# Optimization experiments

Measured on AMD Instinct MI355X. Metric: run time of the kernel, lower is better.

The kernel has to match this reference:

```python
import jax, jax.numpy as jnp
import numpy as np

WH, WW = 7, 7
N = WH * WW
H = 16          # num_heads
D = 32          # head_dim
NW = 64         # num windows per image (mask.shape[0])


def _relative_position_index(wh, ww):
    coords = np.stack(np.meshgrid(np.arange(wh), np.arange(ww), indexing='ij'))  # (2, wh, ww)
    cf = coords.reshape(2, -1)                                                   # (2, N)
    rel = cf[:, :, None] - cf[:, None, :]                                        # (2, N, N)
    rel = rel.transpose(1, 2, 0).copy()
    rel[:, :, 0] += wh - 1
    rel[:, :, 1] += ww - 1
    rel[:, :, 0] *= 2 * ww - 1
    return rel.sum(-1)  # (N, N) int

REL_IDX = jnp.asarray(_relative_position_index(WH, WW))


def setup_inputs() -> dict:
    key = jax.random.key(0)
    ks = jax.random.split(key, 5)
    B_ = 2048
    dim = H * D
    x = jax.random.normal(ks[0], (B_, N, dim), dtype=jnp.float32)
    mask = jnp.zeros((NW, N, N), dtype=jnp.float32)
    rpb_table = jax.random.normal(ks[1], ((2 * WH - 1) * (2 * WW - 1), H), dtype=jnp.float32) * 0.02
    qkv_w = jax.random.normal(ks[2], (3 * dim, dim), dtype=jnp.float32) * (dim ** -0.5)
    qkv_b = jnp.zeros((3 * dim,), dtype=jnp.float32)
    proj_w = jax.random.normal(ks[3], (dim, dim), dtype=jnp.float32) * (dim ** -0.5)
    proj_b = jnp.zeros((dim,), dtype=jnp.float32)
    return {"x": x, "mask": mask, "rpb_table": rpb_table,
            "qkv_w": qkv_w, "qkv_b": qkv_b, "proj_w": proj_w, "proj_b": proj_b}


def reference(x, mask, rpb_table, qkv_w, qkv_b, proj_w, proj_b):
    B_, n, C = x.shape
    scale = D ** -0.5
    # qkv projection (torch Linear: x @ W^T + b)
    qkv = (x @ qkv_w.T + qkv_b).reshape(B_, n, 3, H, D)
    q = qkv[:, :, 0].transpose(0, 2, 1, 3) * scale  # (B_, H, N, D)
    k = qkv[:, :, 1].transpose(0, 2, 1, 3)
    v = qkv[:, :, 2].transpose(0, 2, 1, 3)
    attn = jnp.einsum('bhnd,bhmd->bhnm', q, k)      # (B_, H, N, N)
    # relative position bias: gather (N*N,) rows from table -> (N, N, H) -> (H, N, N)
    bias = rpb_table[REL_IDX.reshape(-1)].reshape(n, n, H).transpose(2, 0, 1)
    attn = attn + bias[None]
    # shifted-window mask add: (B, nW, H, N, N) + (1, nW, 1, N, N)
    nW = mask.shape[0]
    attn = attn.reshape(B_ // nW, nW, H, n, n) + mask[None, :, None]
    attn = attn.reshape(B_, H, n, n)
    attn = jax.nn.softmax(attn, axis=-1)
    out = jnp.einsum('bhnm,bhmd->bhnd', attn, v)    # (B_, H, N, D)
    out = out.transpose(0, 2, 1, 3).reshape(B_, n, H * D)
    return out @ proj_w.T + proj_b
```

## Files before the change

kernel.cpp:

```cpp
#include <hip/hip_runtime.h>

typedef _Float16 f16;
typedef _Float16 f16x8 __attribute__((ext_vector_type(8)));
typedef _Float16 f16x4 __attribute__((ext_vector_type(4)));
typedef __fp16 fp16x2 __attribute__((ext_vector_type(2)));
typedef float f32x4 __attribute__((ext_vector_type(4)));

#define NTOK 49
#define NH 16
#define HD 32
#define DIM 512
#define NWIN 64
#define NB 2048
#define MTOT (NB*NTOK)
#define SCALE 0.17677669529663687f
#define VTS 56

__device__ __forceinline__ void gload_lds16(const f16* g, f16* l) {
    __builtin_amdgcn_global_load_lds((const __attribute__((address_space(1))) void*)g,
                                     (__attribute__((address_space(3))) void*)l, 16, 0, 0);
}

__device__ __forceinline__ void cvt_body(const float* __restrict__ s, f16* __restrict__ d,
                                         int n4, int bid, int nb) {
    int i = bid * 256 + threadIdx.x;
    int st = nb * 256;
    for (; i < n4; i += st) {
        float4 v = ((const float4*)s)[i];
        f16x4 o = { (f16)v.x, (f16)v.y, (f16)v.z, (f16)v.w };
        *(f16x4*)(d + (size_t)i * 4) = o;
    }
}

__global__ __launch_bounds__(256) void prep_kernel(const float* __restrict__ rpb,
                                                   const float* __restrict__ mask,
                                                   f16* __restrict__ biasT,
                                                   f16* __restrict__ maskT,
                                                   const float* __restrict__ qkvw,
                                                   f16* __restrict__ w16,
                                                   const float* __restrict__ projw,
                                                   f16* __restrict__ pw16,
                                                   const float* __restrict__ x,
                                                   f16* __restrict__ x16) {
    const int bid = blockIdx.x;
    if (bid >= 1280) {
        if (bid < 1280 + 2048)      cvt_body(x, x16, MTOT * DIM / 4, bid - 1280, 2048);
        else if (bid < 1280 + 2816) cvt_body(qkvw, w16, 1536 * 512 / 4, bid - 1280 - 2048, 768);
        else                        cvt_body(projw, pw16, 512 * 512 / 4, bid - 1280 - 2816, 256);
        return;
    }
    const bool isBias = (bid < 256);
    int idx = (isBias ? bid : bid - 256) * 256 + threadIdx.x;
    int r  = idx & 3;
    int j  = (idx >> 2) & 3;
    int i  = (idx >> 4) & 3;
    int l  = (idx >> 6) & 63;
    int wh = idx >> 12;
    int g = l >> 4, c16 = l & 15;
    int k = i * 16 + g * 4 + r;
    int q = j * 16 + c16;
    float v;
    if (isBias) {
        if (k >= NTOK)      v = -30000.f;
        else if (q >= NTOK) v = 0.f;
        else {
            int rq = q / 7, cq = q - rq * 7;
            int rk = k / 7, ck = k - rk * 7;
            int rel = (rq - rk + 6) * 13 + (cq - ck + 6);
            v = rpb[rel * NH + wh];
        }
        biasT[idx] = (f16)v;
    } else {
        v = (k < NTOK && q < NTOK) ? mask[(wh * NTOK + q) * NTOK + k] : 0.f;
        maskT[idx] = (f16)v;
    }
}

#define WAIT_LGKM  asm volatile("s_waitcnt lgkmcnt(0)" ::: "memory")
#define WAIT_VM(N) asm volatile("s_waitcnt vmcnt(" #N ")" ::: "memory")

template<int NT>
__global__ __launch_bounds__(512) void gemm256(const f16* __restrict__ A,
                                               const f16* __restrict__ Bw,
                                               const float* __restrict__ bias,
                                               f16* __restrict__ qo,
                                               f16* __restrict__ ko,
                                               f16* __restrict__ vto) {
    __shared__ __align__(16) f16 As[2][256][64];
    __shared__ __align__(16) f16 Bs[2][256][64];

    const int tid = threadIdx.x;
    const int lane = tid & 63;
    const int wv = tid >> 6;
    const int wm = wv >> 2, wn = wv & 3;
    const int g = lane >> 4, c16 = lane & 15;

    const int nblk = gridDim.x;
    const int f = blockIdx.x;
    const int work = (f & 7) * (nblk >> 3) + (f >> 3);
    const int m0 = (work / NT) * 256;
    const int n0 = (work % NT) * 256;

    const int srow = lane >> 3;
    const int schunk = (lane & 7) ^ srow;
    const f16* gA = A  + (size_t)(m0 + wv * 16 + srow) * DIM + schunk * 8;
    const f16* gB = Bw + (size_t)(n0 + wv * 16 + srow) * DIM + schunk * 8;

#define STAGE1(buf, kt, role) do {                                             \
    const f16* _s = (((role) < 2) ? gA : gB) + (size_t)(((role) & 1) * 128) * DIM + (kt) * 64; \
    f16* _d = ((role) < 2) ? &As[buf][((role) & 1) * 128 + wv * 16][0]         \
                           : &Bs[buf][((role) & 1) * 128 + wv * 16][0];        \
    gload_lds16(_s, _d);                                                       \
    gload_lds16(_s + (size_t)8 * DIM, _d + 8 * 64);                            \
} while (0)
#define STAGE_T(buf, kt) do { STAGE1(buf, kt, 0); STAGE1(buf, kt, 1);          \
                              STAGE1(buf, kt, 2); STAGE1(buf, kt, 3); } while (0)

#define READS(buf, kk, AF, BF) do {                                            \
    _Pragma("unroll") for (int _i = 0; _i < 8; ++_i)                           \
        (AF)[_i] = *(const f16x8*)&As[buf][wm * 128 + _i * 16 + c16][(((kk) * 4 + g) ^ (c16 & 7)) * 8]; \
    _Pragma("unroll") for (int _j = 0; _j < 4; ++_j)                           \
        (BF)[_j] = *(const f16x8*)&Bs[buf][wn * 64 + _j * 16 + c16][(((kk) * 4 + g) ^ (c16 & 7)) * 8]; \
} while (0)

#define MM(AF, BF) do {                                                        \
    __builtin_amdgcn_s_setprio(1);                                             \
    _Pragma("unroll") for (int _j = 0; _j < 4; ++_j)                           \
    _Pragma("unroll") for (int _i = 0; _i < 8; ++_i)                           \
        acc[_j][_i] = __builtin_amdgcn_mfma_f32_16x16x32_f16((BF)[_j], (AF)[_i], acc[_j][_i], 0, 0, 0); \
    __builtin_amdgcn_s_setprio(0);                                             \
} while (0)

    f32x4 acc[4][8];
#pragma unroll
    for (int j = 0; j < 4; ++j)
#pragma unroll
        for (int i = 0; i < 8; ++i)
            acc[j][i] = (f32x4){0.f, 0.f, 0.f, 0.f};

    f16x8 a0[8], b0[4], a1[8], b1[4];

    const int KT = DIM / 64;

    STAGE_T(0, 0);
    STAGE_T(1, 1);
    WAIT_VM(8);
    __builtin_amdgcn_s_barrier();
    READS(0, 0, a0, b0);

#pragma unroll
    for (int t = 0; t < KT; ++t) {
        const int b = t & 1, nb = b ^ 1;

        READS(b, 1, a1, b1);
        MM(a0, b0);
        WAIT_LGKM;
        __builtin_amdgcn_s_barrier();
        if (t + 2 < KT) STAGE_T(b, t + 2);
        if (t + 2 < KT) { WAIT_VM(8); }
        else if (t + 1 < KT) { WAIT_VM(0); }

        if (t + 1 < KT) READS(nb, 0, a0, b0);
        MM(a1, b1);
    }
#undef STAGE1
#undef STAGE_T
#undef READS
#undef MM

#pragma unroll
    for (int i = 0; i < 8; ++i) {
        const int m = m0 + wm * 128 + i * 16 + c16;
        const int bb = m / NTOK, tk = m - (m / NTOK) * NTOK;
#pragma unroll
        for (int j = 0; j < 4; ++j) {
            const int n = n0 + wn * 64 + j * 16 + g * 4;
            f32x4 v = acc[j][i];
            const f32x4 b4 = *(const f32x4*)&bias[n];
            v += b4;
            const int s = n >> 9;
            const int hh = (n >> 5) & 15;
            const int d0 = n & 31;
            const size_t bh = (size_t)(bb * NH + hh);
            if (s == 0) {
                f16x4 o = { (f16)(v[0] * SCALE), (f16)(v[1] * SCALE),
                            (f16)(v[2] * SCALE), (f16)(v[3] * SCALE) };
                *(f16x4*)(qo + (bh * NTOK + tk) * HD + d0) = o;
            } else if (s == 1) {
                f16x4 o = { (f16)v[0], (f16)v[1], (f16)v[2], (f16)v[3] };
                *(f16x4*)(ko + (bh * NTOK + tk) * HD + d0) = o;
            } else {
#pragma unroll
                for (int r = 0; r < 4; ++r)
                    vto[(bh * HD + d0 + r) * VTS + tk] = (f16)v[r];
            }
        }
    }
}

__global__ __launch_bounds__(256, 3) void gemm128(const f16* __restrict__ A,
                                                  const f16* __restrict__ Bw,
                                                  const float* __restrict__ bias,
                                                  float* __restrict__ outp) {
    __shared__ __align__(16) f16 As[3][128][32];
    __shared__ __align__(16) f16 Bs[3][128][32];

    const int NT = 4;
    const int tid = threadIdx.x;
    const int lane = tid & 63;
    const int wv = tid >> 6;
    const int wr = wv >> 1, wc = wv & 1;
    const int g = lane >> 4, c16 = lane & 15;
    const int rsw = (c16 >> 1) & 3;

    const int nblk = gridDim.x;
    const int f = blockIdx.x;
    const int work = (f & 7) * (nblk >> 3) + (f >> 3);
    const int m0 = (work / NT) * 128;
    const int n0 = (work % NT) * 128;

    const int srow = lane >> 2;
    const int schunk = (lane & 3) ^ ((srow >> 1) & 3);
    const f16* gA = A  + (size_t)(m0 + wv * 32 + srow) * DIM + schunk * 8;
    const f16* gB = Bw + (size_t)(n0 + wv * 32 + srow) * DIM + schunk * 8;

#define STAGE6(buf, t) do { \
    gload_lds16(gA + (t) * 32,                     &As[buf][wv * 32][0]);      \
    gload_lds16(gA + (size_t)16 * DIM + (t) * 32,  &As[buf][wv * 32 + 16][0]); \
    gload_lds16(gB + (t) * 32,                     &Bs[buf][wv * 32][0]);      \
    gload_lds16(gB + (size_t)16 * DIM + (t) * 32,  &Bs[buf][wv * 32 + 16][0]); \
} while (0)

    f32x4 acc[4][4];
#pragma unroll
    for (int j = 0; j < 4; ++j)
#pragma unroll
        for (int i = 0; i < 4; ++i)
            acc[j][i] = (f32x4){0.f, 0.f, 0.f, 0.f};

    STAGE6(0, 0);
    STAGE6(1, 1);
    WAIT_VM(4);
    __builtin_amdgcn_s_barrier();

    const int KS = DIM / 32;
#pragma unroll
    for (int t = 0; t < KS; ++t) {
        const int cb = t % 3;
        if (t + 2 < KS) STAGE6((t + 2) % 3, t + 2);
        f16x8 af[4], bf[4];
#pragma unroll
        for (int i = 0; i < 4; ++i)
            af[i] = *(const f16x8*)&As[cb][wr * 64 + i * 16 + c16][(g ^ rsw) * 8];
#pragma unroll
        for (int j = 0; j < 4; ++j)
            bf[j] = *(const f16x8*)&Bs[cb][wc * 64 + j * 16 + c16][(g ^ rsw) * 8];
        __builtin_amdgcn_s_setprio(1);
#pragma unroll
        for (int j = 0; j < 4; ++j)
#pragma unroll
            for (int i = 0; i < 4; ++i)
                acc[j][i] = __builtin_amdgcn_mfma_f32_16x16x32_f16(bf[j], af[i], acc[j][i], 0, 0, 0);
        __builtin_amdgcn_s_setprio(0);
        WAIT_LGKM;
        __builtin_amdgcn_sched_barrier(0);
        if (t + 2 < KS) {
            WAIT_VM(4);
        } else if (t + 1 < KS) {
            WAIT_VM(0);
        }
        if (t + 1 < KS) __builtin_amdgcn_s_barrier();
    }
#undef STAGE6

#pragma unroll
    for (int i = 0; i < 4; ++i) {
        const int m = m0 + wr * 64 + i * 16 + c16;
#pragma unroll
        for (int j = 0; j < 4; ++j) {
            const int n = n0 + wc * 64 + j * 16 + g * 4;
            f32x4 v = acc[j][i];
            const f32x4 b4 = *(const f32x4*)&bias[n];
            v += b4;
            float4 o = { v[0], v[1], v[2], v[3] };
            *(float4*)(outp + (size_t)m * DIM + n) = o;
        }
    }
}

__global__ __launch_bounds__(256) void attn_kernel(const f16* __restrict__ qw,
                                                   const f16* __restrict__ kw,
                                                   const f16* __restrict__ vt,
                                                   const f16* __restrict__ biasT,
                                                   const f16* __restrict__ maskT,
                                                   f16* __restrict__ aout) {
    __shared__ __align__(16) f16 Ps[4][64][72];

    const int wv = threadIdx.x >> 6;
    const int l = threadIdx.x & 63;
    const int f = blockIdx.x;
    const int work = (f & 7) * (gridDim.x >> 3) + (f >> 3);
    const int bid = work * 4 + wv;
    const int b = bid >> 4, h = bid & 15;
    const int w = b & (NWIN - 1);
    const int g = l >> 4, c16 = l & 15;
    const size_t qkbase = (size_t)bid * (NTOK * HD);
    const size_t vbase = (size_t)bid * (HD * VTS);

    const f16x8 z8 = {};

    f16x8 qf[4], kf[4];
#pragma unroll
    for (int t = 0; t < 4; ++t) {
        int row = t * 16 + c16;
        f16x8 q = z8, k = z8;
        if (row < NTOK) {
            q = *(const f16x8*)(qw + qkbase + row * HD + g * 8);
            k = *(const f16x8*)(kw + qkbase + row * HD + g * 8);
        }
        qf[t] = q; kf[t] = k;
    }

    const f16* cbB = biasT + (((size_t)h * 64 + l) << 6);
    const f16* cbM = maskT + (((size_t)w * 64 + l) << 6);
    f16x8 cbv[8];
#pragma unroll
    for (int k = 0; k < 8; ++k)
        cbv[k] = *(const f16x8*)(cbB + k * 8) + *(const f16x8*)(cbM + k * 8);
    f32x4 St[4][4];
#pragma unroll
    for (int i = 0; i < 4; ++i)
#pragma unroll
        for (int j = 0; j < 4; ++j) {
            const int e = i * 16 + j * 4;
#pragma unroll
            for (int r = 0; r < 4; ++r)
                St[i][j][r] = (float)cbv[(e + r) >> 3][(e + r) & 7];
        }
#pragma unroll
    for (int i = 0; i < 4; ++i)
#pragma unroll
        for (int j = 0; j < 4; ++j)
            St[i][j] = __builtin_amdgcn_mfma_f32_16x16x32_f16(kf[i], qf[j], St[i][j], 0, 0, 0);

    f16x8 vfp[2][2];
#pragma unroll
    for (int c = 0; c < 2; ++c) {
        int tcol = c * 32 + g * 8;
#pragma unroll
        for (int td = 0; td < 2; ++td) {
            f16x8 vv = z8;
            if (tcol < VTS)
                vv = *(const f16x8*)(vt + vbase + (size_t)(td * 16 + c16) * VTS + tcol);
            vfp[c][td] = vv;
        }
    }

    float inv[4];
#pragma unroll
    for (int j = 0; j < 4; ++j) {
        float m = St[0][j][0];
#pragma unroll
        for (int i = 0; i < 4; ++i)
#pragma unroll
            for (int r = 0; r < 4; ++r) m = fmaxf(m, St[i][j][r]);
        m = fmaxf(m, __shfl_xor(m, 16, 64));
        m = fmaxf(m, __shfl_xor(m, 32, 64));
        float s = 0.f;
#pragma unroll
        for (int i = 0; i < 4; ++i)
#pragma unroll
            for (int r = 0; r < 4; ++r) {
                float p = __expf(St[i][j][r] - m);
                St[i][j][r] = p;
                s += p;
            }
        s += __shfl_xor(s, 16, 64);
        s += __shfl_xor(s, 32, 64);
        inv[j] = 1.f / s;
    }

#pragma unroll
    for (int j = 0; j < 4; ++j) {
        const int q = j * 16 + c16;
#pragma unroll
        for (int i = 0; i < 4; ++i) {
            fp16x2 u0 = __builtin_amdgcn_cvt_pkrtz(St[i][j][0], St[i][j][1]);
            fp16x2 u1 = __builtin_amdgcn_cvt_pkrtz(St[i][j][2], St[i][j][3]);
            *(fp16x2*)&Ps[wv][q][i * 16 + 4 * g]     = u0;
            *(fp16x2*)&Ps[wv][q][i * 16 + 4 * g + 2] = u1;
        }
    }
    WAIT_LGKM;

    f32x4 O2[2][4];
    const f32x4 zf = (f32x4){0.f, 0.f, 0.f, 0.f};
#pragma unroll
    for (int td = 0; td < 2; ++td)
#pragma unroll
        for (int ti = 0; ti < 4; ++ti) O2[td][ti] = zf;
#pragma unroll
    for (int c = 0; c < 2; ++c) {
        f16x8 pf[4];
#pragma unroll
        for (int ti = 0; ti < 4; ++ti)
            pf[ti] = *(const f16x8*)&Ps[wv][ti * 16 + c16][c * 32 + g * 8];
#pragma unroll
        for (int td = 0; td < 2; ++td)
#pragma unroll
            for (int ti = 0; ti < 4; ++ti)
                O2[td][ti] = __builtin_amdgcn_mfma_f32_16x16x32_f16(vfp[c][td], pf[ti], O2[td][ti], 0, 0, 0);
    }

#pragma unroll
    for (int ti = 0; ti < 4; ++ti) {
        int tok = ti * 16 + c16;
        if (tok < NTOK) {
            size_t ob = ((size_t)(b * NTOK + tok)) * DIM + h * HD;
#pragma unroll
            for (int td = 0; td < 2; ++td) {
                f32x4 v = O2[td][ti];
                float iv = inv[ti];
                f16x4 o = { (f16)(v[0] * iv), (f16)(v[1] * iv),
                            (f16)(v[2] * iv), (f16)(v[3] * iv) };
                *(f16x4*)(aout + ob + td * 16 + g * 4) = o;
            }
        }
    }
}

extern "C" void kernel_launch(void* const* d_in, const int* in_sizes, int n_in,
                              void* d_out, int out_size, void* d_ws, size_t ws_size,
                              hipStream_t stream) {
    const float* x      = (const float*)d_in[0];
    const float* mask   = (const float*)d_in[1];
    const float* rpb    = (const float*)d_in[2];
    const float* qkv_w  = (const float*)d_in[3];
    const float* qkv_b  = (const float*)d_in[4];
    const float* proj_w = (const float*)d_in[5];
    const float* proj_b = (const float*)d_in[6];
    float* out = (float*)d_out;

    char* ws = (char*)d_ws;
    size_t o = 0;
    f16* x16   = (f16*)(ws + o); o += (size_t)MTOT * DIM * 2;
    f16* w16   = (f16*)(ws + o); o += (size_t)1536 * 512 * 2;
    f16* pw16  = (f16*)(ws + o); o += (size_t)512 * 512 * 2;
    f16* qws   = (f16*)(ws + o); o += (size_t)NB * NH * NTOK * HD * 2;
    f16* kws   = (f16*)(ws + o); o += (size_t)NB * NH * NTOK * HD * 2;
    f16* vtws  = (f16*)(ws + o); o += (size_t)NB * NH * HD * VTS * 2;
    f16* bT    = (f16*)(ws + o); o += (size_t)NH * 64 * 64 * 2;
    f16* mT    = (f16*)(ws + o); o += (size_t)NWIN * 64 * 64 * 2;
    f16* aout = x16;

    prep_kernel<<<dim3(1280 + 2048 + 768 + 256), dim3(256), 0, stream>>>(
        rpb, mask, bT, mT, qkv_w, w16, proj_w, pw16, x, x16);

    gemm256<6><<<dim3((MTOT / 256) * 6), dim3(512), 0, stream>>>(
        x16, w16, qkv_b, qws, kws, vtws);

    attn_kernel<<<dim3(NB * NH / 4), dim3(256), 0, stream>>>(qws, kws, vtws, bT, mT, aout);

    gemm128<<<dim3((MTOT / 128) * 4), dim3(256), 0, stream>>>(
        aout, pw16, proj_b, out);
}
```

Before: 535.5 us.

## Fuse window attention with output projection in one per-window kernel

Attention and the output projection now run in one kernel. Each 1024-thread block handles one window with all 16 heads, one wave per head. The attention output for the window is kept in a swizzled LDS tile, and each wave then computes 32 output columns of the projection, streaming proj weight fragments straight from global memory. This removes the f16 attention-output round trip through HBM and one kernel launch. In exchange, every block rereads the full 512x512 projection weight from cache without LDS staging, and the large block size plus 147KB of LDS may limit occupancy.

```diff
diff --git a/kernel.cpp b/kernel.cpp
--- a/kernel.cpp
+++ b/kernel.cpp
@@ -198,150 +198,65 @@
     }
 }
 
-__global__ __launch_bounds__(256, 3) void gemm128(const f16* __restrict__ A,
-                                                  const f16* __restrict__ Bw,
-                                                  const float* __restrict__ bias,
-                                                  float* __restrict__ outp) {
-    __shared__ __align__(16) f16 As[3][128][32];
-    __shared__ __align__(16) f16 Bs[3][128][32];
-
-    const int NT = 4;
-    const int tid = threadIdx.x;
-    const int lane = tid & 63;
-    const int wv = tid >> 6;
-    const int wr = wv >> 1, wc = wv & 1;
-    const int g = lane >> 4, c16 = lane & 15;
-    const int rsw = (c16 >> 1) & 3;
-
-    const int nblk = gridDim.x;
-    const int f = blockIdx.x;
-    const int work = (f & 7) * (nblk >> 3) + (f >> 3);
-    const int m0 = (work / NT) * 128;
-    const int n0 = (work % NT) * 128;
-
-    const int srow = lane >> 2;
-    const int schunk = (lane & 3) ^ ((srow >> 1) & 3);
-    const f16* gA = A  + (size_t)(m0 + wv * 32 + srow) * DIM + schunk * 8;
-    const f16* gB = Bw + (size_t)(n0 + wv * 32 + srow) * DIM + schunk * 8;
-
-#define STAGE6(buf, t) do { \
-    gload_lds16(gA + (t) * 32,                     &As[buf][wv * 32][0]);      \
-    gload_lds16(gA + (size_t)16 * DIM + (t) * 32,  &As[buf][wv * 32 + 16][0]); \
-    gload_lds16(gB + (t) * 32,                     &Bs[buf][wv * 32][0]);      \
-    gload_lds16(gB + (size_t)16 * DIM + (t) * 32,  &Bs[buf][wv * 32 + 16][0]); \
-} while (0)
-
-    f32x4 acc[4][4];
-#pragma unroll
-    for (int j = 0; j < 4; ++j)
-#pragma unroll
-        for (int i = 0; i < 4; ++i)
-            acc[j][i] = (f32x4){0.f, 0.f, 0.f, 0.f};
-
-    STAGE6(0, 0);
-    STAGE6(1, 1);
-    WAIT_VM(4);
-    __builtin_amdgcn_s_barrier();
-
-    const int KS = DIM / 32;
-#pragma unroll
-    for (int t = 0; t < KS; ++t) {
-        const int cb = t % 3;
-        if (t + 2 < KS) STAGE6((t + 2) % 3, t + 2);
-        f16x8 af[4], bf[4];
-#pragma unroll
-        for (int i = 0; i < 4; ++i)
-            af[i] = *(const f16x8*)&As[cb][wr * 64 + i * 16 + c16][(g ^ rsw) * 8];
-#pragma unroll
-        for (int j = 0; j < 4; ++j)
-            bf[j] = *(const f16x8*)&Bs[cb][wc * 64 + j * 16 + c16][(g ^ rsw) * 8];
-        __builtin_amdgcn_s_setprio(1);
-#pragma unroll
-        for (int j = 0; j < 4; ++j)
-#pragma unroll
-            for (int i = 0; i < 4; ++i)
-                acc[j][i] = __builtin_amdgcn_mfma_f32_16x16x32_f16(bf[j], af[i], acc[j][i], 0, 0, 0);
-        __builtin_amdgcn_s_setprio(0);
-        WAIT_LGKM;
-        __builtin_amdgcn_sched_barrier(0);
-        if (t + 2 < KS) {
-            WAIT_VM(4);
-        } else if (t + 1 < KS) {
-            WAIT_VM(0);
-        }
-        if (t + 1 < KS) __builtin_amdgcn_s_barrier();
-    }
-#undef STAGE6
-
-#pragma unroll
-    for (int i = 0; i < 4; ++i) {
-        const int m = m0 + wr * 64 + i * 16 + c16;
-#pragma unroll
-        for (int j = 0; j < 4; ++j) {
-            const int n = n0 + wc * 64 + j * 16 + g * 4;
-            f32x4 v = acc[j][i];
-            const f32x4 b4 = *(const f32x4*)&bias[n];
-            v += b4;
-            float4 o = { v[0], v[1], v[2], v[3] };
-            *(float4*)(outp + (size_t)m * DIM + n) = o;
-        }
-    }
-}
-
-__global__ __launch_bounds__(256) void attn_kernel(const f16* __restrict__ qw,
-                                                   const f16* __restrict__ kw,
-                                                   const f16* __restrict__ vt,
-                                                   const f16* __restrict__ biasT,
-                                                   const f16* __restrict__ maskT,
-                                                   f16* __restrict__ aout) {
-    __shared__ __align__(16) f16 Ps[4][64][72];
-
-    const int wv = threadIdx.x >> 6;
+__global__ __launch_bounds__(1024, 4) void attn_proj_kernel(const f16* __restrict__ qw,
+                                                            const f16* __restrict__ kw,
+                                                            const f16* __restrict__ vt,
+                                                            const f16* __restrict__ biasT,
+                                                            const f16* __restrict__ maskT,
+                                                            const f16* __restrict__ pw16,
+                                                            const float* __restrict__ projb,
+                                                            float* __restrict__ outp) {
+    __shared__ __align__(16) f16 Ps[16][64][72];
+    f16* act = &Ps[0][0][0];
+
+    const int h = threadIdx.x >> 6;
     const int l = threadIdx.x & 63;
     const int f = blockIdx.x;
-    const int work = (f & 7) * (gridDim.x >> 3) + (f >> 3);
-    const int bid = work * 4 + wv;
-    const int b = bid >> 4, h = bid & 15;
+    const int b = (f & 7) * (gridDim.x >> 3) + (f >> 3);
     const int w = b & (NWIN - 1);
     const int g = l >> 4, c16 = l & 15;
+    const int bid = b * NH + h;
     const size_t qkbase = (size_t)bid * (NTOK * HD);
     const size_t vbase = (size_t)bid * (HD * VTS);
 
     const f16x8 z8 = {};
 
-    f16x8 qf[4], kf[4];
-#pragma unroll
-    for (int t = 0; t < 4; ++t) {
-        int row = t * 16 + c16;
-        f16x8 q = z8, k = z8;
-        if (row < NTOK) {
-            q = *(const f16x8*)(qw + qkbase + row * HD + g * 8);
-            k = *(const f16x8*)(kw + qkbase + row * HD + g * 8);
-        }
-        qf[t] = q; kf[t] = k;
-    }
-
     const f16* cbB = biasT + (((size_t)h * 64 + l) << 6);
     const f16* cbM = maskT + (((size_t)w * 64 + l) << 6);
-    f16x8 cbv[8];
-#pragma unroll
-    for (int k = 0; k < 8; ++k)
-        cbv[k] = *(const f16x8*)(cbB + k * 8) + *(const f16x8*)(cbM + k * 8);
     f32x4 St[4][4];
-#pragma unroll
-    for (int i = 0; i < 4; ++i)
-#pragma unroll
-        for (int j = 0; j < 4; ++j) {
-            const int e = i * 16 + j * 4;
-#pragma unroll
-            for (int r = 0; r < 4; ++r)
-                St[i][j][r] = (float)cbv[(e + r) >> 3][(e + r) & 7];
-        }
-#pragma unroll
-    for (int i = 0; i < 4; ++i)
-#pragma unroll
-        for (int j = 0; j < 4; ++j)
-            St[i][j] = __builtin_amdgcn_mfma_f32_16x16x32_f16(kf[i], qf[j], St[i][j], 0, 0, 0);
+    {
+        f16x8 cbv[8];
+#pragma unroll
+        for (int k = 0; k < 8; ++k)
+            cbv[k] = *(const f16x8*)(cbB + k * 8) + *(const f16x8*)(cbM + k * 8);
+#pragma unroll
+        for (int i = 0; i < 4; ++i)
+#pragma unroll
+            for (int j = 0; j < 4; ++j) {
+                const int e = i * 16 + j * 4;
+#pragma unroll
+                for (int r = 0; r < 4; ++r)
+                    St[i][j][r] = (float)cbv[(e + r) >> 3][(e + r) & 7];
+            }
+    }
+    {
+        f16x8 qf[4], kf[4];
+#pragma unroll
+        for (int t = 0; t < 4; ++t) {
+            int row = t * 16 + c16;
+            f16x8 q = z8, k = z8;
+            if (row < NTOK) {
+                q = *(const f16x8*)(qw + qkbase + row * HD + g * 8);
+                k = *(const f16x8*)(kw + qkbase + row * HD + g * 8);
+            }
+            qf[t] = q; kf[t] = k;
+        }
+#pragma unroll
+        for (int i = 0; i < 4; ++i)
+#pragma unroll
+            for (int j = 0; j < 4; ++j)
+                St[i][j] = __builtin_amdgcn_mfma_f32_16x16x32_f16(kf[i], qf[j], St[i][j], 0, 0, 0);
+    }
 
     f16x8 vfp[2][2];
 #pragma unroll
@@ -387,8 +302,8 @@
         for (int i = 0; i < 4; ++i) {
             fp16x2 u0 = __builtin_amdgcn_cvt_pkrtz(St[i][j][0], St[i][j][1]);
             fp16x2 u1 = __builtin_amdgcn_cvt_pkrtz(St[i][j][2], St[i][j][3]);
-            *(fp16x2*)&Ps[wv][q][i * 16 + 4 * g]     = u0;
-            *(fp16x2*)&Ps[wv][q][i * 16 + 4 * g + 2] = u1;
+            *(fp16x2*)&Ps[h][q][i * 16 + 4 * g]     = u0;
+            *(fp16x2*)&Ps[h][q][i * 16 + 4 * g + 2] = u1;
         }
     }
     WAIT_LGKM;
@@ -404,26 +319,87 @@
         f16x8 pf[4];
 #pragma unroll
         for (int ti = 0; ti < 4; ++ti)
-            pf[ti] = *(const f16x8*)&Ps[wv][ti * 16 + c16][c * 32 + g * 8];
+            pf[ti] = *(const f16x8*)&Ps[h][ti * 16 + c16][c * 32 + g * 8];
 #pragma unroll
         for (int td = 0; td < 2; ++td)
 #pragma unroll
             for (int ti = 0; ti < 4; ++ti)
                 O2[td][ti] = __builtin_amdgcn_mfma_f32_16x16x32_f16(vfp[c][td], pf[ti], O2[td][ti], 0, 0, 0);
     }
+
+    __syncthreads();
 
 #pragma unroll
     for (int ti = 0; ti < 4; ++ti) {
         int tok = ti * 16 + c16;
         if (tok < NTOK) {
-            size_t ob = ((size_t)(b * NTOK + tok)) * DIM + h * HD;
 #pragma unroll
             for (int td = 0; td < 2; ++td) {
                 f32x4 v = O2[td][ti];
                 float iv = inv[ti];
                 f16x4 o = { (f16)(v[0] * iv), (f16)(v[1] * iv),
                             (f16)(v[2] * iv), (f16)(v[3] * iv) };
-                *(f16x4*)(aout + ob + td * 16 + g * 4) = o;
+                int col = h * 32 + td * 16 + g * 4;
+                int chunk = (col >> 3) ^ (tok & 7);
+                *(f16x4*)((char*)act + tok * 1024 + (chunk << 4) + (col & 7) * 2) = o;
+            }
+        }
+    }
+    if (l < 60) {
+        int row = 49 + (l >> 2);
+        int chunk = (h * 4 + (l & 3)) ^ (row & 7);
+        *(f16x8*)((char*)act + row * 1024 + (chunk << 4)) = z8;
+    }
+    __syncthreads();
+
+    f32x4 pacc[2][4];
+#pragma unroll
+    for (int j = 0; j < 2; ++j)
+#pragma unroll
+        for (int i = 0; i < 4; ++i) pacc[j][i] = zf;
+
+    const f16* gW0 = pw16 + (size_t)(h * 32 + c16) * DIM + g * 8;
+    f16x8 bfc[2];
+#pragma unroll
+    for (int j = 0; j < 2; ++j)
+        bfc[j] = *(const f16x8*)(gW0 + (size_t)(j * 16) * DIM);
+
+#pragma unroll
+    for (int ks = 0; ks < 16; ++ks) {
+        f16x8 af[4];
+#pragma unroll
+        for (int i = 0; i < 4; ++i) {
+            int m = i * 16 + c16;
+            int chunk = (ks * 4 + g) ^ (m & 7);
+            af[i] = *(const f16x8*)((char*)act + m * 1024 + (chunk << 4));
+        }
+        f16x8 bfn[2];
+        if (ks + 1 < 16) {
+#pragma unroll
+            for (int j = 0; j < 2; ++j)
+                bfn[j] = *(const f16x8*)(gW0 + (size_t)(j * 16) * DIM + (ks + 1) * 32);
+        }
+        __builtin_amdgcn_s_setprio(1);
+#pragma unroll
+        for (int j = 0; j < 2; ++j)
+#pragma unroll
+            for (int i = 0; i < 4; ++i)
+                pacc[j][i] = __builtin_amdgcn_mfma_f32_16x16x32_f16(bfc[j], af[i], pacc[j][i], 0, 0, 0);
+        __builtin_amdgcn_s_setprio(0);
+        bfc[0] = bfn[0]; bfc[1] = bfn[1];
+    }
+
+#pragma unroll
+    for (int i = 0; i < 4; ++i) {
+        const int m = i * 16 + c16;
+        if (m < NTOK) {
+#pragma unroll
+            for (int j = 0; j < 2; ++j) {
+                const int n = h * 32 + j * 16 + g * 4;
+                f32x4 v = pacc[j][i];
+                v += *(const f32x4*)&projb[n];
+                float4 o = { v[0], v[1], v[2], v[3] };
+                *(float4*)(outp + ((size_t)(b * NTOK + m)) * DIM + n) = o;
             }
         }
     }
@@ -451,7 +427,6 @@
     f16* vtws  = (f16*)(ws + o); o += (size_t)NB * NH * HD * VTS * 2;
     f16* bT    = (f16*)(ws + o); o += (size_t)NH * 64 * 64 * 2;
     f16* mT    = (f16*)(ws + o); o += (size_t)NWIN * 64 * 64 * 2;
-    f16* aout = x16;
 
     prep_kernel<<<dim3(1280 + 2048 + 768 + 256), dim3(256), 0, stream>>>(
         rpb, mask, bT, mT, qkv_w, w16, proj_w, pw16, x, x16);
@@ -459,8 +434,6 @@
     gemm256<6><<<dim3((MTOT / 256) * 6), dim3(512), 0, stream>>>(
         x16, w16, qkv_b, qws, kws, vtws);
 
-    attn_kernel<<<dim3(NB * NH / 4), dim3(256), 0, stream>>>(qws, kws, vtws, bT, mT, aout);
-
-    gemm128<<<dim3((MTOT / 128) * 4), dim3(256), 0, stream>>>(
-        aout, pw16, proj_b, out);
-}
+    attn_proj_kernel<<<dim3(NB), dim3(1024), 0, stream>>>(
+        qws, kws, vtws, bT, mT, pw16, proj_b, out);
+}
```

New measurement: 552.7 us. +3.2%, slower.
